# Optimization experiments

Hardware: AMD Instinct MI355X
Metric: run time of the kernel (lower is better)

## Reference

```python
import jax, jax.numpy as jnp
import numpy as np

B, S, D_IN, D_OUT, H = 2, 2048, 1024, 1024, 16
HD = D_OUT // H


def setup_inputs() -> dict:
    key = jax.random.key(0)
    ks = jax.random.split(key, 6)
    s = 0.02
    return {
        "X": jax.random.normal(ks[0], (B, S, D_IN), dtype=jnp.float32),
        "Wq": jax.random.normal(ks[1], (D_OUT, D_IN), dtype=jnp.float32) * s,
        "Wk": jax.random.normal(ks[2], (D_OUT, D_IN), dtype=jnp.float32) * s,
        "Wv": jax.random.normal(ks[3], (D_OUT, D_IN), dtype=jnp.float32) * s,
        "Wo": jax.random.normal(ks[4], (D_OUT, D_OUT), dtype=jnp.float32) * s,
        "bo": jax.random.normal(ks[5], (D_OUT,), dtype=jnp.float32) * s,
    }


def reference(X, Wq, Wk, Wv, Wo, bo):
    b, n, _ = X.shape
    # torch Linear: y = x @ W^T
    Q = (X @ Wq.T).reshape(b, n, H, HD).transpose(0, 2, 1, 3)  # [b,h,s,hd]
    K = (X @ Wk.T).reshape(b, n, H, HD).transpose(0, 2, 1, 3)
    V = (X @ Wv.T).reshape(b, n, H, HD).transpose(0, 2, 1, 3)
    S_ = jnp.einsum('bhqd,bhkd->bhqk', Q, K)  # [b,h,s,s]
    causal = jnp.triu(jnp.ones((n, n), dtype=bool), k=1)
    S_ = jnp.where(causal, -jnp.inf, S_)
    W = jax.nn.softmax(S_ / jnp.sqrt(jnp.float32(HD)), axis=-1)
    Z = jnp.einsum('bhqk,bhkd->bhqd', W, V)
    Z = Z.transpose(0, 2, 1, 3).reshape(b, n, D_OUT)
    return Z @ Wo.T + bo
```

## Files before the change

### kernel.cpp

```cpp
#include <hip/hip_runtime.h>
#include <stdint.h>

typedef __bf16 bf16x8 __attribute__((ext_vector_type(8)));
typedef float  f32x4  __attribute__((ext_vector_type(4)));
typedef unsigned int u32x4 __attribute__((ext_vector_type(4)));

#define S_   2048
#define DM   1024
#define QSCALE 0.18033688011112042f

__device__ __forceinline__ unsigned short f2b(float f) {
    uint32_t u = __builtin_bit_cast(uint32_t, f);
    u += 0x7fffu + ((u >> 16) & 1u);
    return (unsigned short)(u >> 16);
}

__device__ __forceinline__ uint32_t pack2bf(float a, float b) {
    uint32_t ua = __builtin_bit_cast(uint32_t, a) + 0x8000u;
    uint32_t ub = __builtin_bit_cast(uint32_t, b) + 0x8000u;
    return __builtin_amdgcn_perm(ub, ua, 0x07060302);
}

__device__ __forceinline__ void glds16(const void* g, void* l) {
    __builtin_amdgcn_global_load_lds(
        (const __attribute__((address_space(1))) void*)g,
        (__attribute__((address_space(3))) void*)l, 16, 0, 0);
}

__global__ void cvt_all(const float* __restrict__ X,
                        const float* __restrict__ Wq, const float* __restrict__ Wk,
                        const float* __restrict__ Wv,
                        unsigned short* __restrict__ Xb, unsigned short* __restrict__ Wb)
{
    size_t i = ((size_t)blockIdx.x * 256 + threadIdx.x) * 4;
    const float* src;
    unsigned short* dst;
    size_t off;
    if (i < (size_t)4194304) { src = X; dst = Xb; off = i; }
    else {
        size_t j = i - 4194304;
        int sel = (int)(j >> 20);
        off = j & 1048575;
        src = (sel == 0) ? Wq : (sel == 1) ? Wk : Wv;
        dst = Wb + (size_t)sel * 1048576;
    }
    float4 v = *(const float4*)&src[off];
    uint2 o;
    o.x = pack2bf(v.x, v.y);
    o.y = pack2bf(v.z, v.w);
    *(uint2*)&dst[off] = o;
}

__global__ void cvt_wo(const float* __restrict__ Wo, unsigned short* __restrict__ Wob)
{
    size_t i = ((size_t)blockIdx.x * 256 + threadIdx.x) * 4;
    float4 v = *(const float4*)&Wo[i];
    uint2 o;
    o.x = pack2bf(v.x, v.y);
    o.y = pack2bf(v.z, v.w);
    *(uint2*)&Wob[i] = o;
}

__global__ __launch_bounds__(256, 2)
void qkv_gemm(const unsigned short* __restrict__ Xb,
              const unsigned short* __restrict__ Wqb,
              const unsigned short* __restrict__ Wkb,
              const unsigned short* __restrict__ Wvb,
              unsigned short* __restrict__ Qo, unsigned short* __restrict__ Ko,
              unsigned short* __restrict__ Vto)
{
    __shared__ unsigned short Ash[128 * 32];
    __shared__ unsigned short Bsh[128 * 32];

    const int t = threadIdx.x;
    const int lane = t & 63, w = t >> 6;
    const int lcol = lane & 15, quad = lane >> 4;
    const int z = blockIdx.z;
    const int rowBase = ((z == 2) ? blockIdx.x : blockIdx.y) * 128;
    const int colBase = ((z == 2) ? blockIdx.y : blockIdx.x) * 128;
    const unsigned short* aPtr = (z == 2) ? Wvb : Xb;
    const unsigned short* bPtr = (z == 0) ? Wqb : (z == 1) ? Wkb : Xb;
    const int wr = (w >> 1) * 64, wc = (w & 1) * 64;

    f32x4 acc[4][4];
    #pragma unroll
    for (int i = 0; i < 4; ++i)
        #pragma unroll
        for (int j = 0; j < 4; ++j) acc[i][j] = (f32x4){0.f,0.f,0.f,0.f};

    for (int k0 = 0; k0 < DM; k0 += 32) {
        __syncthreads();
        #pragma unroll
        for (int p = 0; p < 2; ++p) {
            int ci = p * 256 + t;
            glds16(&aPtr[(size_t)(rowBase + (ci >> 2)) * DM + k0 + (ci & 3) * 8], &Ash[ci * 8]);
        }
        #pragma unroll
        for (int p = 0; p < 2; ++p) {
            int ci = p * 256 + t;
            glds16(&bPtr[(size_t)(colBase + (ci >> 2)) * DM + k0 + (ci & 3) * 8], &Bsh[ci * 8]);
        }
        __syncthreads();
        bf16x8 af[4], bfr[4];
        #pragma unroll
        for (int i = 0; i < 4; ++i) af[i]  = *(const bf16x8*)&Ash[(wr + i*16 + lcol)*32 + quad*8];
        #pragma unroll
        for (int i = 0; i < 4; ++i) bfr[i] = *(const bf16x8*)&Bsh[(wc + i*16 + lcol)*32 + quad*8];
        #pragma unroll
        for (int i = 0; i < 4; ++i)
            #pragma unroll
            for (int j = 0; j < 4; ++j)
                acc[i][j] = __builtin_amdgcn_mfma_f32_16x16x32_bf16(af[i], bfr[j], acc[i][j], 0, 0, 0);
    }

    unsigned short* Cm = (z == 0) ? Qo : (z == 1) ? Ko : Vto;
    const int ld = (z == 2) ? (S_ * 2) : DM;
    const float sc = (z == 0) ? QSCALE : 1.0f;
    #pragma unroll
    for (int i = 0; i < 4; ++i)
        #pragma unroll
        for (int j = 0; j < 4; ++j)
            #pragma unroll
            for (int r = 0; r < 4; ++r) {
                int row = rowBase + wr + i*16 + quad*4 + r;
                int col = colBase + wc + j*16 + lcol;
                Cm[(size_t)row * ld + col] = f2b(acc[i][j][r] * sc);
            }
}

__global__ __launch_bounds__(512, 4)
void attn_kernel(const unsigned short* __restrict__ Q,
                 const unsigned short* __restrict__ K,
                 const unsigned short* __restrict__ Vt,
                 unsigned short* __restrict__ Z)
{
    __shared__ __align__(16) unsigned short SH[18432];

    const int t = threadIdx.x;
    const int lane = t & 63, w = t >> 6;
    const int lcol = lane & 15, quad = lane >> 4;
    const int kh = w & 1, wq = w >> 1;

    const int bh = blockIdx.x;
    const int b = bh >> 4, h = bh & 15;
    const int y = blockIdx.y;
    const int tile = (y < 8) ? (15 - y) : (y - 8);
    const int q0 = tile * 128;
    const int nchunk = 2 * tile + 2;

    const unsigned short* Qg = Q + (size_t)(b * S_ + q0) * DM + h * 64;
    const unsigned short* Kg = K + (size_t)(b * S_) * DM + h * 64;
    const unsigned short* Vg = Vt + (size_t)(h * 64) * (S_ * 2) + b * S_;

    bf16x8 qf[2][2];
    #pragma unroll
    for (int qi = 0; qi < 2; ++qi)
        #pragma unroll
        for (int kd = 0; kd < 2; ++kd)
            qf[qi][kd] = *(const bf16x8*)&Qg[(size_t)(wq*32 + qi*16 + lcol) * DM + kd*32 + quad*8];

    bool mk[4];
    #pragma unroll
    for (int r = 0; r < 4; ++r) mk[r] = (quad*4 + r) > lcol;

    float lp[2] = {0.f, 0.f};
    f32x4 o[2][4];
    #pragma unroll
    for (int qi = 0; qi < 2; ++qi)
        #pragma unroll
        for (int nd = 0; nd < 4; ++nd) o[qi][nd] = (f32x4){0.f,0.f,0.f,0.f};

    const int sr = t >> 3, sch = t & 7;

    {
        uint4 k0 = *(const uint4*)&Kg[(size_t)sr * DM + sch * 8];
        uint4 v0 = *(const uint4*)&Vg[(size_t)sr * (S_ * 2) + sch * 8];
        *(uint4*)&SH[sr * 72 + sch * 8] = k0;
        *(uint4*)&SH[9216 + sr * 72 + sch * 8] = v0;
    }
    __syncthreads();

    const int Qb0 = tile * 8 + wq * 2;
    const int gq = ((quad & 1) << 1) | (quad >> 1);
    const bool qodd = (quad & 1) != 0;

    for (int c = 0; c < nchunk; ++c) {
        const int cur = c & 1;
        const bool pf = (c + 1 < nchunk);
        uint4 kn, vn;
        if (pf) {
            const int kc1 = (c + 1) * 64;
            kn = *(const uint4*)&Kg[(size_t)(kc1 + sr) * DM + sch * 8];
            vn = *(const uint4*)&Vg[(size_t)sr * (S_ * 2) + kc1 + sch * 8];
        }
        const unsigned short* Kc = &SH[cur * 4608];
        const unsigned short* Vc = &SH[9216 + cur * 4608];

        const int Kb0 = c * 4 + kh * 2;
        if (Kb0 <= Qb0 + 1) {
            uint32_t pw[2][2][2];
            #pragma unroll
            for (int nk = 0; nk < 2; ++nk) {
                const int Kb = Kb0 + nk;
                if (Kb <= Qb0 + 1) {
                    bf16x8 ak0 = *(const bf16x8*)&Kc[(kh*32 + nk*16 + lcol)*72 + quad*8];
                    bf16x8 ak1 = *(const bf16x8*)&Kc[(kh*32 + nk*16 + lcol)*72 + 32 + quad*8];
                    #pragma unroll
                    for (int qi = 0; qi < 2; ++qi) {
                        if (Kb <= Qb0 + qi) {
                            f32x4 s = (f32x4){0.f,0.f,0.f,0.f};
                            s = __builtin_amdgcn_mfma_f32_16x16x32_bf16(ak0, qf[qi][0], s, 0, 0, 0);
                            s = __builtin_amdgcn_mfma_f32_16x16x32_bf16(ak1, qf[qi][1], s, 0, 0, 0);
                            float p0 = __builtin_amdgcn_exp2f(s[0]);
                            float p1 = __builtin_amdgcn_exp2f(s[1]);
                            float p2 = __builtin_amdgcn_exp2f(s[2]);
                            float p3 = __builtin_amdgcn_exp2f(s[3]);
                            if (Kb == Qb0 + qi) {
                                p0 = mk[0] ? 0.f : p0;
                                p1 = mk[1] ? 0.f : p1;
                                p2 = mk[2] ? 0.f : p2;
                                p3 = mk[3] ? 0.f : p3;
                            }
                            lp[qi] += (p0 + p1) + (p2 + p3);
                            pw[qi][nk][0] = pack2bf(p0, p1);
                            pw[qi][nk][1] = pack2bf(p2, p3);
                        } else {
                            pw[qi][nk][0] = 0u;
                            pw[qi][nk][1] = 0u;
                        }
                    }
                } else {
                    #pragma unroll
                    for (int qi = 0; qi < 2; ++qi) {
                        pw[qi][nk][0] = 0u;
                        pw[qi][nk][1] = 0u;
                    }
                }
            }

            bf16x8 ap[2];
            #pragma unroll
            for (int qi = 0; qi < 2; ++qi) {
                uint32_t a0 = pw[qi][0][0], a1 = pw[qi][0][1];
                uint32_t b0 = pw[qi][1][0], b1 = pw[qi][1][1];
                uint32_t xa0 = (uint32_t)__shfl_xor((int)a0, 16);
                uint32_t xa1 = (uint32_t)__shfl_xor((int)a1, 16);
                uint32_t xb0 = (uint32_t)__shfl_xor((int)b0, 16);
                uint32_t xb1 = (uint32_t)__shfl_xor((int)b1, 16);
                u32x4 apw;
                apw[0] = qodd ? xb0 : a0;
                apw[1] = qodd ? xb1 : a1;
                apw[2] = qodd ? b0 : xa0;
                apw[3] = qodd ? b1 : xa1;
                ap[qi] = __builtin_bit_cast(bf16x8, apw);
            }

            #pragma unroll
            for (int nd = 0; nd < 4; ++nd) {
                bf16x8 bv = *(const bf16x8*)&Vc[(nd*16 + lcol)*72 + kh*32 + gq*8];
                #pragma unroll
                for (int qi = 0; qi < 2; ++qi)
                    o[qi][nd] = __builtin_amdgcn_mfma_f32_16x16x32_bf16(ap[qi], bv, o[qi][nd], 0, 0, 0);
            }
        }

        if (pf) {
            *(uint4*)&SH[(cur ^ 1) * 4608 + sr * 72 + sch * 8] = kn;
            *(uint4*)&SH[9216 + (cur ^ 1) * 4608 + sr * 72 + sch * 8] = vn;
        }
        __syncthreads();
    }

    #pragma unroll
    for (int qi = 0; qi < 2; ++qi) {
        lp[qi] += __shfl_xor(lp[qi], 16);
        lp[qi] += __shfl_xor(lp[qi], 32);
    }
    float* red = (float*)SH;
    float* my = red + (wq * 64 + lane) * 36;
    if (kh == 1) {
        #pragma unroll
        for (int qi = 0; qi < 2; ++qi)
            #pragma unroll
            for (int nd = 0; nd < 4; ++nd)
                *(f32x4*)&my[qi*16 + nd*4] = o[qi][nd];
        my[32] = lp[0];
        my[33] = lp[1];
    }
    __syncthreads();
    if (kh == 0) {
        #pragma unroll
        for (int qi = 0; qi < 2; ++qi)
            #pragma unroll
            for (int nd = 0; nd < 4; ++nd)
                o[qi][nd] += *(const f32x4*)&my[qi*16 + nd*4];
        float linv[2];
        linv[0] = 1.0f / (lp[0] + my[32]);
        linv[1] = 1.0f / (lp[1] + my[33]);
        #pragma unroll
        for (int qi = 0; qi < 2; ++qi)
            #pragma unroll
            for (int r = 0; r < 4; ++r) {
                float lr = __shfl(linv[qi], quad*4 + r);
                unsigned short* Zr = Z + (size_t)(b*S_ + q0 + wq*32 + qi*16 + quad*4 + r) * DM + h*64;
                #pragma unroll
                for (int nd = 0; nd < 4; ++nd)
                    Zr[nd*16 + lcol] = f2b(o[qi][nd][r] * lr);
            }
    }
}

__global__ __launch_bounds__(256, 4)
void out_gemm(const unsigned short* __restrict__ A,
              const unsigned short* __restrict__ Wob, const float* __restrict__ bo,
              float* __restrict__ Out)
{
    __shared__ unsigned short Ash[64 * 32];
    __shared__ unsigned short Bsh[128 * 32];

    const int t = threadIdx.x;
    const int lane = t & 63, w = t >> 6;
    const int lcol = lane & 15, quad = lane >> 4;
    const int rowBase = blockIdx.y * 64;
    const int colBase = blockIdx.x * 128;
    const int wr = (w >> 1) * 32, wc = (w & 1) * 64;

    f32x4 acc[2][4];
    #pragma unroll
    for (int i = 0; i < 2; ++i)
        #pragma unroll
        for (int j = 0; j < 4; ++j) acc[i][j] = (f32x4){0.f,0.f,0.f,0.f};

    for (int k0 = 0; k0 < DM; k0 += 32) {
        __syncthreads();
        glds16(&A[(size_t)(rowBase + (t >> 2)) * DM + k0 + (t & 3) * 8], &Ash[t * 8]);
        #pragma unroll
        for (int p = 0; p < 2; ++p) {
            int ci = p * 256 + t;
            glds16(&Wob[(size_t)(colBase + (ci >> 2)) * DM + k0 + (ci & 3) * 8], &Bsh[ci * 8]);
        }
        __syncthreads();
        bf16x8 af[2], bfr[4];
        #pragma unroll
        for (int i = 0; i < 2; ++i) af[i]  = *(const bf16x8*)&Ash[(wr + i*16 + lcol)*32 + quad*8];
        #pragma unroll
        for (int j = 0; j < 4; ++j) bfr[j] = *(const bf16x8*)&Bsh[(wc + j*16 + lcol)*32 + quad*8];
        #pragma unroll
        for (int i = 0; i < 2; ++i)
            #pragma unroll
            for (int j = 0; j < 4; ++j)
                acc[i][j] = __builtin_amdgcn_mfma_f32_16x16x32_bf16(af[i], bfr[j], acc[i][j], 0, 0, 0);
    }

    float bb[4];
    #pragma unroll
    for (int j = 0; j < 4; ++j) bb[j] = bo[colBase + wc + j*16 + lcol];

    #pragma unroll
    for (int i = 0; i < 2; ++i)
        #pragma unroll
        for (int j = 0; j < 4; ++j)
            #pragma unroll
            for (int r = 0; r < 4; ++r) {
                int row = rowBase + wr + i*16 + quad*4 + r;
                int col = colBase + wc + j*16 + lcol;
                Out[(size_t)row * DM + col] = acc[i][j][r] + bb[j];
            }
}

extern "C" void kernel_launch(void* const* d_in, const int* in_sizes, int n_in,
                              void* d_out, int out_size, void* d_ws, size_t ws_size,
                              hipStream_t stream) {
    const float* X  = (const float*)d_in[0];
    const float* Wq = (const float*)d_in[1];
    const float* Wk = (const float*)d_in[2];
    const float* Wv = (const float*)d_in[3];
    const float* Wo = (const float*)d_in[4];
    const float* bo = (const float*)d_in[5];
    float* out = (float*)d_out;

    unsigned short* Xb  = (unsigned short*)d_ws;
    unsigned short* Qw  = Xb + (size_t)4096 * 1024;
    unsigned short* Kw  = Qw + (size_t)4096 * 1024;
    unsigned short* Vtw = Kw + (size_t)4096 * 1024;
    unsigned short* Zb  = Xb;
    unsigned short* Wob = Qw;
    unsigned short* Wb  = (unsigned short*)d_out;

    cvt_all<<<dim3(7168), 256, 0, stream>>>(X, Wq, Wk, Wv, Xb, Wb);
    qkv_gemm<<<dim3(8, 32, 3), 256, 0, stream>>>(Xb, Wb, Wb + (size_t)1048576,
                                                 Wb + (size_t)2097152, Qw, Kw, Vtw);
    attn_kernel<<<dim3(32, 16), 512, 0, stream>>>(Qw, Kw, Vtw, Zb);
    cvt_wo<<<dim3(1024), 256, 0, stream>>>(Wo, Wob);
    out_gemm<<<dim3(8, 64), 256, 0, stream>>>(Zb, Wob, bo, out);
}
```

Baseline: 179.1 us.

## Halve attention query tile to 64 rows and use 16x16x16 MFMA for PV

Shrinks the attention block from 512 to 256 threads with 64-row query tiles, doubling the grid and adjusting the causal chunk count and K/V staging loops. When the 16x16x16 bf16 MFMA builtin is available, the P·V product uses it directly on the packed probability registers, avoiding the cross-lane shuffles that repack P for the 16x16x32 instruction. The aim is better load balance and occupancy on the causal workload with less shuffle overhead. The cost is K/V being reloaded by twice as many blocks and twice as many smaller-K MFMAs.

```diff
diff --git a/kernel.cpp b/kernel.cpp
--- a/kernel.cpp
+++ b/kernel.cpp
@@ -3,6 +3,8 @@
 
 typedef __bf16 bf16x8 __attribute__((ext_vector_type(8)));
 typedef float  f32x4  __attribute__((ext_vector_type(4)));
+typedef short  s16x4  __attribute__((ext_vector_type(4)));
+typedef unsigned int u32x2 __attribute__((ext_vector_type(2)));
 typedef unsigned int u32x4 __attribute__((ext_vector_type(4)));
 
 #define S_   2048
@@ -128,7 +130,13 @@
             }
 }
 
-__global__ __launch_bounds__(512, 4)
+#if __has_builtin(__builtin_amdgcn_mfma_f32_16x16x16bf16_1k)
+#define PV16 1
+#else
+#define PV16 0
+#endif
+
+__global__ __launch_bounds__(256, 4)
 void attn_kernel(const unsigned short* __restrict__ Q,
                  const unsigned short* __restrict__ K,
                  const unsigned short* __restrict__ Vt,
@@ -144,9 +152,9 @@
     const int bh = blockIdx.x;
     const int b = bh >> 4, h = bh & 15;
     const int y = blockIdx.y;
-    const int tile = (y < 8) ? (15 - y) : (y - 8);
-    const int q0 = tile * 128;
-    const int nchunk = 2 * tile + 2;
+    const int tile = (y < 16) ? (31 - y) : (y - 16);
+    const int q0 = tile * 64;
+    const int nchunk = tile + 1;
 
     const unsigned short* Qg = Q + (size_t)(b * S_ + q0) * DM + h * 64;
     const unsigned short* Kg = K + (size_t)(b * S_) * DM + h * 64;
@@ -172,26 +180,34 @@
 
     const int sr = t >> 3, sch = t & 7;
 
-    {
-        uint4 k0 = *(const uint4*)&Kg[(size_t)sr * DM + sch * 8];
-        uint4 v0 = *(const uint4*)&Vg[(size_t)sr * (S_ * 2) + sch * 8];
-        *(uint4*)&SH[sr * 72 + sch * 8] = k0;
-        *(uint4*)&SH[9216 + sr * 72 + sch * 8] = v0;
+    #pragma unroll
+    for (int p = 0; p < 2; ++p) {
+        const int row = p*32 + sr;
+        uint4 k0 = *(const uint4*)&Kg[(size_t)row * DM + sch * 8];
+        uint4 v0 = *(const uint4*)&Vg[(size_t)row * (S_ * 2) + sch * 8];
+        *(uint4*)&SH[row * 72 + sch * 8] = k0;
+        *(uint4*)&SH[9216 + row * 72 + sch * 8] = v0;
     }
     __syncthreads();
 
-    const int Qb0 = tile * 8 + wq * 2;
+    const int Qb0 = tile * 4 + wq * 2;
+#if !PV16
     const int gq = ((quad & 1) << 1) | (quad >> 1);
     const bool qodd = (quad & 1) != 0;
+#endif
 
     for (int c = 0; c < nchunk; ++c) {
         const int cur = c & 1;
         const bool pf = (c + 1 < nchunk);
-        uint4 kn, vn;
+        uint4 kn[2], vn[2];
         if (pf) {
             const int kc1 = (c + 1) * 64;
-            kn = *(const uint4*)&Kg[(size_t)(kc1 + sr) * DM + sch * 8];
-            vn = *(const uint4*)&Vg[(size_t)sr * (S_ * 2) + kc1 + sch * 8];
+            #pragma unroll
+            for (int p = 0; p < 2; ++p) {
+                const int row = p*32 + sr;
+                kn[p] = *(const uint4*)&Kg[(size_t)(kc1 + row) * DM + sch * 8];
+                vn[p] = *(const uint4*)&Vg[(size_t)row * (S_ * 2) + kc1 + sch * 8];
+            }
         }
         const unsigned short* Kc = &SH[cur * 4608];
         const unsigned short* Vc = &SH[9216 + cur * 4608];
@@ -238,6 +254,26 @@
                 }
             }
 
+#if PV16
+            #pragma unroll
+            for (int nk = 0; nk < 2; ++nk) {
+                if (Kb0 + nk <= Qb0 + 1) {
+                    #pragma unroll
+                    for (int nd = 0; nd < 4; ++nd) {
+                        s16x4 bv = *(const s16x4*)&Vc[(nd*16 + lcol)*72 + kh*32 + nk*16 + quad*4];
+                        #pragma unroll
+                        for (int qi = 0; qi < 2; ++qi) {
+                            u32x2 wv;
+                            wv[0] = pw[qi][nk][0];
+                            wv[1] = pw[qi][nk][1];
+                            s16x4 ap = __builtin_bit_cast(s16x4, wv);
+                            o[qi][nd] = __builtin_amdgcn_mfma_f32_16x16x16bf16_1k(
+                                            ap, bv, o[qi][nd], 0, 0, 0);
+                        }
+                    }
+                }
+            }
+#else
             bf16x8 ap[2];
             #pragma unroll
             for (int qi = 0; qi < 2; ++qi) {
@@ -254,7 +290,6 @@
                 apw[3] = qodd ? b1 : xa1;
                 ap[qi] = __builtin_bit_cast(bf16x8, apw);
             }
-
             #pragma unroll
             for (int nd = 0; nd < 4; ++nd) {
                 bf16x8 bv = *(const bf16x8*)&Vc[(nd*16 + lcol)*72 + kh*32 + gq*8];
@@ -262,11 +297,16 @@
                 for (int qi = 0; qi < 2; ++qi)
                     o[qi][nd] = __builtin_amdgcn_mfma_f32_16x16x32_bf16(ap[qi], bv, o[qi][nd], 0, 0, 0);
             }
+#endif
         }
 
         if (pf) {
-            *(uint4*)&SH[(cur ^ 1) * 4608 + sr * 72 + sch * 8] = kn;
-            *(uint4*)&SH[9216 + (cur ^ 1) * 4608 + sr * 72 + sch * 8] = vn;
+            #pragma unroll
+            for (int p = 0; p < 2; ++p) {
+                const int row = p*32 + sr;
+                *(uint4*)&SH[(cur ^ 1) * 4608 + row * 72 + sch * 8] = kn[p];
+                *(uint4*)&SH[9216 + (cur ^ 1) * 4608 + row * 72 + sch * 8] = vn[p];
+            }
         }
         __syncthreads();
     }
@@ -390,7 +430,7 @@
     cvt_all<<<dim3(7168), 256, 0, stream>>>(X, Wq, Wk, Wv, Xb, Wb);
     qkv_gemm<<<dim3(8, 32, 3), 256, 0, stream>>>(Xb, Wb, Wb + (size_t)1048576,
                                                  Wb + (size_t)2097152, Qw, Kw, Vtw);
-    attn_kernel<<<dim3(32, 16), 512, 0, stream>>>(Qw, Kw, Vtw, Zb);
+    attn_kernel<<<dim3(32, 32), 256, 0, stream>>>(Qw, Kw, Vtw, Zb);
     cvt_wo<<<dim3(1024), 256, 0, stream>>>(Wo, Wob);
     out_gemm<<<dim3(8, 64), 256, 0, stream>>>(Zb, Wob, bo, out);
 }
```

New measurement: 217.5 us. 1.21x slower.

## Double attention key chunk size to 128 and add MFMA priority hints

Applied to the files above, without the earlier changes.

The attention kernel now processes 128 keys per chunk instead of 64. Each key-half wave handles four 16-key blocks and splits the PV product into two 32-key passes. This halves the number of loop iterations and block-wide barriers per tile, and LDS use nearly doubles to hold the larger K and V double buffers. s_setprio hints are also wrapped around the MFMA groups, which may reduce occupancy and adds more register pressure from the larger prefetch registers.

```diff
diff --git a/kernel.cpp b/kernel.cpp
--- a/kernel.cpp
+++ b/kernel.cpp
@@ -134,7 +134,7 @@
                  const unsigned short* __restrict__ Vt,
                  unsigned short* __restrict__ Z)
 {
-    __shared__ __align__(16) unsigned short SH[18432];
+    __shared__ __align__(16) unsigned short SH[35840];
 
     const int t = threadIdx.x;
     const int lane = t & 63, w = t >> 6;
@@ -146,7 +146,7 @@
     const int y = blockIdx.y;
     const int tile = (y < 8) ? (15 - y) : (y - 8);
     const int q0 = tile * 128;
-    const int nchunk = 2 * tile + 2;
+    const int nchunk = tile + 1;
 
     const unsigned short* Qg = Q + (size_t)(b * S_ + q0) * DM + h * 64;
     const unsigned short* Kg = K + (size_t)(b * S_) * DM + h * 64;
@@ -171,12 +171,17 @@
         for (int nd = 0; nd < 4; ++nd) o[qi][nd] = (f32x4){0.f,0.f,0.f,0.f};
 
     const int sr = t >> 3, sch = t & 7;
+    const int vr = t >> 4, vch = t & 15;
 
     {
-        uint4 k0 = *(const uint4*)&Kg[(size_t)sr * DM + sch * 8];
-        uint4 v0 = *(const uint4*)&Vg[(size_t)sr * (S_ * 2) + sch * 8];
-        *(uint4*)&SH[sr * 72 + sch * 8] = k0;
-        *(uint4*)&SH[9216 + sr * 72 + sch * 8] = v0;
+        uint4 k0a = *(const uint4*)&Kg[(size_t)sr * DM + sch * 8];
+        uint4 k0b = *(const uint4*)&Kg[(size_t)(64 + sr) * DM + sch * 8];
+        uint4 v0a = *(const uint4*)&Vg[(size_t)vr * (S_ * 2) + vch * 8];
+        uint4 v0b = *(const uint4*)&Vg[(size_t)(32 + vr) * (S_ * 2) + vch * 8];
+        *(uint4*)&SH[sr * 72 + sch * 8] = k0a;
+        *(uint4*)&SH[(64 + sr) * 72 + sch * 8] = k0b;
+        *(uint4*)&SH[18432 + vr * 136 + vch * 8] = v0a;
+        *(uint4*)&SH[18432 + (32 + vr) * 136 + vch * 8] = v0b;
     }
     __syncthreads();
 
@@ -187,86 +192,95 @@
     for (int c = 0; c < nchunk; ++c) {
         const int cur = c & 1;
         const bool pf = (c + 1 < nchunk);
-        uint4 kn, vn;
+        uint4 kn[2], vn[2];
         if (pf) {
-            const int kc1 = (c + 1) * 64;
-            kn = *(const uint4*)&Kg[(size_t)(kc1 + sr) * DM + sch * 8];
-            vn = *(const uint4*)&Vg[(size_t)sr * (S_ * 2) + kc1 + sch * 8];
-        }
-        const unsigned short* Kc = &SH[cur * 4608];
-        const unsigned short* Vc = &SH[9216 + cur * 4608];
-
-        const int Kb0 = c * 4 + kh * 2;
-        if (Kb0 <= Qb0 + 1) {
-            uint32_t pw[2][2][2];
-            #pragma unroll
-            for (int nk = 0; nk < 2; ++nk) {
-                const int Kb = Kb0 + nk;
-                if (Kb <= Qb0 + 1) {
-                    bf16x8 ak0 = *(const bf16x8*)&Kc[(kh*32 + nk*16 + lcol)*72 + quad*8];
-                    bf16x8 ak1 = *(const bf16x8*)&Kc[(kh*32 + nk*16 + lcol)*72 + 32 + quad*8];
-                    #pragma unroll
-                    for (int qi = 0; qi < 2; ++qi) {
-                        if (Kb <= Qb0 + qi) {
-                            f32x4 s = (f32x4){0.f,0.f,0.f,0.f};
-                            s = __builtin_amdgcn_mfma_f32_16x16x32_bf16(ak0, qf[qi][0], s, 0, 0, 0);
-                            s = __builtin_amdgcn_mfma_f32_16x16x32_bf16(ak1, qf[qi][1], s, 0, 0, 0);
-                            float p0 = __builtin_amdgcn_exp2f(s[0]);
-                            float p1 = __builtin_amdgcn_exp2f(s[1]);
-                            float p2 = __builtin_amdgcn_exp2f(s[2]);
-                            float p3 = __builtin_amdgcn_exp2f(s[3]);
-                            if (Kb == Qb0 + qi) {
-                                p0 = mk[0] ? 0.f : p0;
-                                p1 = mk[1] ? 0.f : p1;
-                                p2 = mk[2] ? 0.f : p2;
-                                p3 = mk[3] ? 0.f : p3;
-                            }
-                            lp[qi] += (p0 + p1) + (p2 + p3);
-                            pw[qi][nk][0] = pack2bf(p0, p1);
-                            pw[qi][nk][1] = pack2bf(p2, p3);
-                        } else {
-                            pw[qi][nk][0] = 0u;
-                            pw[qi][nk][1] = 0u;
+            const int kc1 = (c + 1) * 128;
+            kn[0] = *(const uint4*)&Kg[(size_t)(kc1 + sr) * DM + sch * 8];
+            kn[1] = *(const uint4*)&Kg[(size_t)(kc1 + 64 + sr) * DM + sch * 8];
+            vn[0] = *(const uint4*)&Vg[(size_t)vr * (S_ * 2) + kc1 + vch * 8];
+            vn[1] = *(const uint4*)&Vg[(size_t)(32 + vr) * (S_ * 2) + kc1 + vch * 8];
+        }
+        const unsigned short* Kc = &SH[cur * 9216];
+        const unsigned short* Vc = &SH[18432 + cur * 8704];
+
+        const int Kb0 = c * 8 + kh * 4;
+        uint32_t pw[2][4][2];
+        #pragma unroll
+        for (int qi = 0; qi < 2; ++qi)
+            #pragma unroll
+            for (int nk = 0; nk < 4; ++nk) {
+                pw[qi][nk][0] = 0u;
+                pw[qi][nk][1] = 0u;
+            }
+
+        #pragma unroll
+        for (int nk = 0; nk < 4; ++nk) {
+            const int Kb = Kb0 + nk;
+            if (Kb <= Qb0 + 1) {
+                bf16x8 ak0 = *(const bf16x8*)&Kc[(kh*64 + nk*16 + lcol)*72 + quad*8];
+                bf16x8 ak1 = *(const bf16x8*)&Kc[(kh*64 + nk*16 + lcol)*72 + 32 + quad*8];
+                #pragma unroll
+                for (int qi = 0; qi < 2; ++qi) {
+                    if (Kb <= Qb0 + qi) {
+                        f32x4 s = (f32x4){0.f,0.f,0.f,0.f};
+                        __builtin_amdgcn_s_setprio(1);
+                        s = __builtin_amdgcn_mfma_f32_16x16x32_bf16(ak0, qf[qi][0], s, 0, 0, 0);
+                        s = __builtin_amdgcn_mfma_f32_16x16x32_bf16(ak1, qf[qi][1], s, 0, 0, 0);
+                        __builtin_amdgcn_s_setprio(0);
+                        float p0 = __builtin_amdgcn_exp2f(s[0]);
+                        float p1 = __builtin_amdgcn_exp2f(s[1]);
+                        float p2 = __builtin_amdgcn_exp2f(s[2]);
+                        float p3 = __builtin_amdgcn_exp2f(s[3]);
+                        if (Kb == Qb0 + qi) {
+                            p0 = mk[0] ? 0.f : p0;
+                            p1 = mk[1] ? 0.f : p1;
+                            p2 = mk[2] ? 0.f : p2;
+                            p3 = mk[3] ? 0.f : p3;
                         }
-                    }
-                } else {
-                    #pragma unroll
-                    for (int qi = 0; qi < 2; ++qi) {
-                        pw[qi][nk][0] = 0u;
-                        pw[qi][nk][1] = 0u;
+                        lp[qi] += (p0 + p1) + (p2 + p3);
+                        pw[qi][nk][0] = pack2bf(p0, p1);
+                        pw[qi][nk][1] = pack2bf(p2, p3);
                     }
                 }
             }
-
-            bf16x8 ap[2];
-            #pragma unroll
-            for (int qi = 0; qi < 2; ++qi) {
-                uint32_t a0 = pw[qi][0][0], a1 = pw[qi][0][1];
-                uint32_t b0 = pw[qi][1][0], b1 = pw[qi][1][1];
-                uint32_t xa0 = (uint32_t)__shfl_xor((int)a0, 16);
-                uint32_t xa1 = (uint32_t)__shfl_xor((int)a1, 16);
-                uint32_t xb0 = (uint32_t)__shfl_xor((int)b0, 16);
-                uint32_t xb1 = (uint32_t)__shfl_xor((int)b1, 16);
-                u32x4 apw;
-                apw[0] = qodd ? xb0 : a0;
-                apw[1] = qodd ? xb1 : a1;
-                apw[2] = qodd ? b0 : xa0;
-                apw[3] = qodd ? b1 : xa1;
-                ap[qi] = __builtin_bit_cast(bf16x8, apw);
-            }
-
-            #pragma unroll
-            for (int nd = 0; nd < 4; ++nd) {
-                bf16x8 bv = *(const bf16x8*)&Vc[(nd*16 + lcol)*72 + kh*32 + gq*8];
+        }
+
+        #pragma unroll
+        for (int pr = 0; pr < 2; ++pr) {
+            if (Kb0 + 2*pr <= Qb0 + 1) {
+                bf16x8 ap[2];
                 #pragma unroll
-                for (int qi = 0; qi < 2; ++qi)
-                    o[qi][nd] = __builtin_amdgcn_mfma_f32_16x16x32_bf16(ap[qi], bv, o[qi][nd], 0, 0, 0);
+                for (int qi = 0; qi < 2; ++qi) {
+                    uint32_t a0 = pw[qi][2*pr][0], a1 = pw[qi][2*pr][1];
+                    uint32_t b0 = pw[qi][2*pr+1][0], b1 = pw[qi][2*pr+1][1];
+                    uint32_t xa0 = (uint32_t)__shfl_xor((int)a0, 16);
+                    uint32_t xa1 = (uint32_t)__shfl_xor((int)a1, 16);
+                    uint32_t xb0 = (uint32_t)__shfl_xor((int)b0, 16);
+                    uint32_t xb1 = (uint32_t)__shfl_xor((int)b1, 16);
+                    u32x4 apw;
+                    apw[0] = qodd ? xb0 : a0;
+                    apw[1] = qodd ? xb1 : a1;
+                    apw[2] = qodd ? b0 : xa0;
+                    apw[3] = qodd ? b1 : xa1;
+                    ap[qi] = __builtin_bit_cast(bf16x8, apw);
+                }
+                #pragma unroll
+                for (int nd = 0; nd < 4; ++nd) {
+                    bf16x8 bv = *(const bf16x8*)&Vc[(nd*16 + lcol)*136 + kh*64 + pr*32 + gq*8];
+                    __builtin_amdgcn_s_setprio(1);
+                    #pragma unroll
+                    for (int qi = 0; qi < 2; ++qi)
+                        o[qi][nd] = __builtin_amdgcn_mfma_f32_16x16x32_bf16(ap[qi], bv, o[qi][nd], 0, 0, 0);
+                    __builtin_amdgcn_s_setprio(0);
+                }
             }
         }
 
         if (pf) {
-            *(uint4*)&SH[(cur ^ 1) * 4608 + sr * 72 + sch * 8] = kn;
-            *(uint4*)&SH[9216 + (cur ^ 1) * 4608 + sr * 72 + sch * 8] = vn;
+            *(uint4*)&SH[(cur ^ 1) * 9216 + sr * 72 + sch * 8] = kn[0];
+            *(uint4*)&SH[(cur ^ 1) * 9216 + (64 + sr) * 72 + sch * 8] = kn[1];
+            *(uint4*)&SH[18432 + (cur ^ 1) * 8704 + vr * 136 + vch * 8] = vn[0];
+            *(uint4*)&SH[18432 + (cur ^ 1) * 8704 + (32 + vr) * 136 + vch * 8] = vn[1];
         }
         __syncthreads();
     }
```

New measurement: 195.9 us. +9.3%, slower.

## Split long causal attention tiles across two blocks with partial-sum combine kernel

Applied to the files above, without the earlier changes.

Rebalances the causal attention work. Each heavy query tile (tiles 8-15) is split at key chunk 17 between two blocks, and the second block then also processes a light tile (0-7). Unnormalized partial outputs and row sums go to scratch (d_out for outputs, unused rows of Z for sums), and a new combine kernel merges them and normalizes. This evens out per-block work and removes the long-tail blocks, at the cost of an extra launch and the fp32 partial-buffer traffic. No running max is needed because the softmax has no max subtraction.

```diff
diff --git a/kernel.cpp b/kernel.cpp
--- a/kernel.cpp
+++ b/kernel.cpp
@@ -132,7 +132,8 @@
 void attn_kernel(const unsigned short* __restrict__ Q,
                  const unsigned short* __restrict__ K,
                  const unsigned short* __restrict__ Vt,
-                 unsigned short* __restrict__ Z)
+                 unsigned short* __restrict__ Z,
+                 float* __restrict__ Part)
 {
     __shared__ __align__(16) unsigned short SH[18432];
 
@@ -144,169 +145,240 @@
     const int bh = blockIdx.x;
     const int b = bh >> 4, h = bh & 15;
     const int y = blockIdx.y;
-    const int tile = (y < 8) ? (15 - y) : (y - 8);
-    const int q0 = tile * 128;
-    const int nchunk = 2 * tile + 2;
-
-    const unsigned short* Qg = Q + (size_t)(b * S_ + q0) * DM + h * 64;
+    const int ab = y >> 3;
+    const int p = y & 7;
+    const int Hv = 15 - p;
+    const int nH = 2 * Hv + 2;
+
     const unsigned short* Kg = K + (size_t)(b * S_) * DM + h * 64;
     const unsigned short* Vg = Vt + (size_t)(h * 64) * (S_ * 2) + b * S_;
 
-    bf16x8 qf[2][2];
-    #pragma unroll
-    for (int qi = 0; qi < 2; ++qi)
-        #pragma unroll
-        for (int kd = 0; kd < 2; ++kd)
-            qf[qi][kd] = *(const bf16x8*)&Qg[(size_t)(wq*32 + qi*16 + lcol) * DM + kd*32 + quad*8];
-
     bool mk[4];
     #pragma unroll
     for (int r = 0; r < 4; ++r) mk[r] = (quad*4 + r) > lcol;
 
-    float lp[2] = {0.f, 0.f};
-    f32x4 o[2][4];
-    #pragma unroll
-    for (int qi = 0; qi < 2; ++qi)
-        #pragma unroll
-        for (int nd = 0; nd < 4; ++nd) o[qi][nd] = (f32x4){0.f,0.f,0.f,0.f};
-
     const int sr = t >> 3, sch = t & 7;
 
-    {
-        uint4 k0 = *(const uint4*)&Kg[(size_t)sr * DM + sch * 8];
-        uint4 v0 = *(const uint4*)&Vg[(size_t)sr * (S_ * 2) + sch * 8];
-        *(uint4*)&SH[sr * 72 + sch * 8] = k0;
-        *(uint4*)&SH[9216 + sr * 72 + sch * 8] = v0;
-    }
-    __syncthreads();
-
-    const int Qb0 = tile * 8 + wq * 2;
     const int gq = ((quad & 1) << 1) | (quad >> 1);
     const bool qodd = (quad & 1) != 0;
 
-    for (int c = 0; c < nchunk; ++c) {
-        const int cur = c & 1;
-        const bool pf = (c + 1 < nchunk);
-        uint4 kn, vn;
-        if (pf) {
-            const int kc1 = (c + 1) * 64;
-            kn = *(const uint4*)&Kg[(size_t)(kc1 + sr) * DM + sch * 8];
-            vn = *(const uint4*)&Vg[(size_t)sr * (S_ * 2) + kc1 + sch * 8];
-        }
-        const unsigned short* Kc = &SH[cur * 4608];
-        const unsigned short* Vc = &SH[9216 + cur * 4608];
-
-        const int Kb0 = c * 4 + kh * 2;
-        if (Kb0 <= Qb0 + 1) {
-            uint32_t pw[2][2][2];
-            #pragma unroll
-            for (int nk = 0; nk < 2; ++nk) {
-                const int Kb = Kb0 + nk;
-                if (Kb <= Qb0 + 1) {
-                    bf16x8 ak0 = *(const bf16x8*)&Kc[(kh*32 + nk*16 + lcol)*72 + quad*8];
-                    bf16x8 ak1 = *(const bf16x8*)&Kc[(kh*32 + nk*16 + lcol)*72 + 32 + quad*8];
-                    #pragma unroll
-                    for (int qi = 0; qi < 2; ++qi) {
-                        if (Kb <= Qb0 + qi) {
-                            f32x4 s = (f32x4){0.f,0.f,0.f,0.f};
-                            s = __builtin_amdgcn_mfma_f32_16x16x32_bf16(ak0, qf[qi][0], s, 0, 0, 0);
-                            s = __builtin_amdgcn_mfma_f32_16x16x32_bf16(ak1, qf[qi][1], s, 0, 0, 0);
-                            float p0 = __builtin_amdgcn_exp2f(s[0]);
-                            float p1 = __builtin_amdgcn_exp2f(s[1]);
-                            float p2 = __builtin_amdgcn_exp2f(s[2]);
-                            float p3 = __builtin_amdgcn_exp2f(s[3]);
-                            if (Kb == Qb0 + qi) {
-                                p0 = mk[0] ? 0.f : p0;
-                                p1 = mk[1] ? 0.f : p1;
-                                p2 = mk[2] ? 0.f : p2;
-                                p3 = mk[3] ? 0.f : p3;
+    const int nseg = (ab == 0) ? 1 : 2;
+    for (int seg = 0; seg < nseg; ++seg) {
+        int tile, c0, c1;
+        bool finalSeg;
+        if (ab == 0)      { tile = Hv; c0 = 0;  c1 = 17;      finalSeg = false; }
+        else if (seg == 0){ tile = Hv; c0 = 17; c1 = nH;      finalSeg = false; }
+        else              { tile = p;  c0 = 0;  c1 = 2*p + 2; finalSeg = true;  }
+
+        const int q0 = tile * 128;
+        const unsigned short* Qg = Q + (size_t)(b * S_ + q0) * DM + h * 64;
+
+        bf16x8 qf[2][2];
+        #pragma unroll
+        for (int qi = 0; qi < 2; ++qi)
+            #pragma unroll
+            for (int kd = 0; kd < 2; ++kd)
+                qf[qi][kd] = *(const bf16x8*)&Qg[(size_t)(wq*32 + qi*16 + lcol) * DM + kd*32 + quad*8];
+
+        float lp[2] = {0.f, 0.f};
+        f32x4 o[2][4];
+        #pragma unroll
+        for (int qi = 0; qi < 2; ++qi)
+            #pragma unroll
+            for (int nd = 0; nd < 4; ++nd) o[qi][nd] = (f32x4){0.f,0.f,0.f,0.f};
+
+        {
+            const int kc0 = c0 * 64;
+            uint4 k0 = *(const uint4*)&Kg[(size_t)(kc0 + sr) * DM + sch * 8];
+            uint4 v0 = *(const uint4*)&Vg[(size_t)sr * (S_ * 2) + kc0 + sch * 8];
+            *(uint4*)&SH[(c0 & 1) * 4608 + sr * 72 + sch * 8] = k0;
+            *(uint4*)&SH[9216 + (c0 & 1) * 4608 + sr * 72 + sch * 8] = v0;
+        }
+        __syncthreads();
+
+        const int Qb0 = tile * 8 + wq * 2;
+
+        for (int c = c0; c < c1; ++c) {
+            const int cur = c & 1;
+            const bool pf = (c + 1 < c1);
+            uint4 kn, vn;
+            if (pf) {
+                const int kc1 = (c + 1) * 64;
+                kn = *(const uint4*)&Kg[(size_t)(kc1 + sr) * DM + sch * 8];
+                vn = *(const uint4*)&Vg[(size_t)sr * (S_ * 2) + kc1 + sch * 8];
+            }
+            const unsigned short* Kc = &SH[cur * 4608];
+            const unsigned short* Vc = &SH[9216 + cur * 4608];
+
+            const int Kb0 = c * 4 + kh * 2;
+            if (Kb0 <= Qb0 + 1) {
+                uint32_t pw[2][2][2];
+                #pragma unroll
+                for (int nk = 0; nk < 2; ++nk) {
+                    const int Kb = Kb0 + nk;
+                    if (Kb <= Qb0 + 1) {
+                        bf16x8 ak0 = *(const bf16x8*)&Kc[(kh*32 + nk*16 + lcol)*72 + quad*8];
+                        bf16x8 ak1 = *(const bf16x8*)&Kc[(kh*32 + nk*16 + lcol)*72 + 32 + quad*8];
+                        #pragma unroll
+                        for (int qi = 0; qi < 2; ++qi) {
+                            if (Kb <= Qb0 + qi) {
+                                f32x4 s = (f32x4){0.f,0.f,0.f,0.f};
+                                s = __builtin_amdgcn_mfma_f32_16x16x32_bf16(ak0, qf[qi][0], s, 0, 0, 0);
+                                s = __builtin_amdgcn_mfma_f32_16x16x32_bf16(ak1, qf[qi][1], s, 0, 0, 0);
+                                float p0 = __builtin_amdgcn_exp2f(s[0]);
+                                float p1 = __builtin_amdgcn_exp2f(s[1]);
+                                float p2 = __builtin_amdgcn_exp2f(s[2]);
+                                float p3 = __builtin_amdgcn_exp2f(s[3]);
+                                if (Kb == Qb0 + qi) {
+                                    p0 = mk[0] ? 0.f : p0;
+                                    p1 = mk[1] ? 0.f : p1;
+                                    p2 = mk[2] ? 0.f : p2;
+                                    p3 = mk[3] ? 0.f : p3;
+                                }
+                                lp[qi] += (p0 + p1) + (p2 + p3);
+                                pw[qi][nk][0] = pack2bf(p0, p1);
+                                pw[qi][nk][1] = pack2bf(p2, p3);
+                            } else {
+                                pw[qi][nk][0] = 0u;
+                                pw[qi][nk][1] = 0u;
                             }
-                            lp[qi] += (p0 + p1) + (p2 + p3);
-                            pw[qi][nk][0] = pack2bf(p0, p1);
-                            pw[qi][nk][1] = pack2bf(p2, p3);
-                        } else {
+                        }
+                    } else {
+                        #pragma unroll
+                        for (int qi = 0; qi < 2; ++qi) {
                             pw[qi][nk][0] = 0u;
                             pw[qi][nk][1] = 0u;
                         }
                     }
-                } else {
+                }
+
+                bf16x8 ap[2];
+                #pragma unroll
+                for (int qi = 0; qi < 2; ++qi) {
+                    uint32_t a0 = pw[qi][0][0], a1 = pw[qi][0][1];
+                    uint32_t b0 = pw[qi][1][0], b1 = pw[qi][1][1];
+                    uint32_t xa0 = (uint32_t)__shfl_xor((int)a0, 16);
+                    uint32_t xa1 = (uint32_t)__shfl_xor((int)a1, 16);
+                    uint32_t xb0 = (uint32_t)__shfl_xor((int)b0, 16);
+                    uint32_t xb1 = (uint32_t)__shfl_xor((int)b1, 16);
+                    u32x4 apw;
+                    apw[0] = qodd ? xb0 : a0;
+                    apw[1] = qodd ? xb1 : a1;
+                    apw[2] = qodd ? b0 : xa0;
+                    apw[3] = qodd ? b1 : xa1;
+                    ap[qi] = __builtin_bit_cast(bf16x8, apw);
+                }
+
+                #pragma unroll
+                for (int nd = 0; nd < 4; ++nd) {
+                    bf16x8 bv = *(const bf16x8*)&Vc[(nd*16 + lcol)*72 + kh*32 + gq*8];
                     #pragma unroll
-                    for (int qi = 0; qi < 2; ++qi) {
-                        pw[qi][nk][0] = 0u;
-                        pw[qi][nk][1] = 0u;
+                    for (int qi = 0; qi < 2; ++qi)
+                        o[qi][nd] = __builtin_amdgcn_mfma_f32_16x16x32_bf16(ap[qi], bv, o[qi][nd], 0, 0, 0);
+                }
+            }
+
+            if (pf) {
+                *(uint4*)&SH[(cur ^ 1) * 4608 + sr * 72 + sch * 8] = kn;
+                *(uint4*)&SH[9216 + (cur ^ 1) * 4608 + sr * 72 + sch * 8] = vn;
+            }
+            __syncthreads();
+        }
+
+        #pragma unroll
+        for (int qi = 0; qi < 2; ++qi) {
+            lp[qi] += __shfl_xor(lp[qi], 16);
+            lp[qi] += __shfl_xor(lp[qi], 32);
+        }
+        float* red = (float*)SH;
+        float* my = red + (wq * 64 + lane) * 36;
+        if (kh == 1) {
+            #pragma unroll
+            for (int qi = 0; qi < 2; ++qi)
+                #pragma unroll
+                for (int nd = 0; nd < 4; ++nd)
+                    *(f32x4*)&my[qi*16 + nd*4] = o[qi][nd];
+            my[32] = lp[0];
+            my[33] = lp[1];
+        }
+        __syncthreads();
+        if (kh == 0) {
+            #pragma unroll
+            for (int qi = 0; qi < 2; ++qi)
+                #pragma unroll
+                for (int nd = 0; nd < 4; ++nd)
+                    o[qi][nd] += *(const f32x4*)&my[qi*16 + nd*4];
+            float ltot[2];
+            ltot[0] = lp[0] + my[32];
+            ltot[1] = lp[1] + my[33];
+
+            if (finalSeg) {
+                float linv[2];
+                linv[0] = 1.0f / ltot[0];
+                linv[1] = 1.0f / ltot[1];
+                #pragma unroll
+                for (int qi = 0; qi < 2; ++qi)
+                    #pragma unroll
+                    for (int r = 0; r < 4; ++r) {
+                        float lr = __shfl(linv[qi], quad*4 + r);
+                        unsigned short* Zr = Z + (size_t)(b*S_ + q0 + wq*32 + qi*16 + quad*4 + r) * DM + h*64;
+                        #pragma unroll
+                        for (int nd = 0; nd < 4; ++nd)
+                            Zr[nd*16 + lcol] = f2b(o[qi][nd][r] * lr);
                     }
+            } else {
+                float* po = Part + (size_t)(ab ? 2097152 : 0) + (size_t)(bh*8 + p) * 8192;
+                #pragma unroll
+                for (int qi = 0; qi < 2; ++qi)
+                    #pragma unroll
+                    for (int nd = 0; nd < 4; ++nd)
+                        #pragma unroll
+                        for (int r = 0; r < 4; ++r)
+                            po[(wq*32 + qi*16 + quad*4 + r)*64 + nd*16 + lcol] = o[qi][nd][r];
+                if (quad == 0) {
+                    float* st = (float*)(Z + (size_t)(b*S_ + Hv*128 + wq + (ab ? 4 : 0)) * DM + h*64);
+                    st[lcol]      = ltot[0];
+                    st[16 + lcol] = ltot[1];
                 }
             }
-
-            bf16x8 ap[2];
-            #pragma unroll
-            for (int qi = 0; qi < 2; ++qi) {
-                uint32_t a0 = pw[qi][0][0], a1 = pw[qi][0][1];
-                uint32_t b0 = pw[qi][1][0], b1 = pw[qi][1][1];
-                uint32_t xa0 = (uint32_t)__shfl_xor((int)a0, 16);
-                uint32_t xa1 = (uint32_t)__shfl_xor((int)a1, 16);
-                uint32_t xb0 = (uint32_t)__shfl_xor((int)b0, 16);
-                uint32_t xb1 = (uint32_t)__shfl_xor((int)b1, 16);
-                u32x4 apw;
-                apw[0] = qodd ? xb0 : a0;
-                apw[1] = qodd ? xb1 : a1;
-                apw[2] = qodd ? b0 : xa0;
-                apw[3] = qodd ? b1 : xa1;
-                ap[qi] = __builtin_bit_cast(bf16x8, apw);
-            }
-
-            #pragma unroll
-            for (int nd = 0; nd < 4; ++nd) {
-                bf16x8 bv = *(const bf16x8*)&Vc[(nd*16 + lcol)*72 + kh*32 + gq*8];
-                #pragma unroll
-                for (int qi = 0; qi < 2; ++qi)
-                    o[qi][nd] = __builtin_amdgcn_mfma_f32_16x16x32_bf16(ap[qi], bv, o[qi][nd], 0, 0, 0);
-            }
-        }
-
-        if (pf) {
-            *(uint4*)&SH[(cur ^ 1) * 4608 + sr * 72 + sch * 8] = kn;
-            *(uint4*)&SH[9216 + (cur ^ 1) * 4608 + sr * 72 + sch * 8] = vn;
         }
         __syncthreads();
     }
-
-    #pragma unroll
-    for (int qi = 0; qi < 2; ++qi) {
-        lp[qi] += __shfl_xor(lp[qi], 16);
-        lp[qi] += __shfl_xor(lp[qi], 32);
-    }
-    float* red = (float*)SH;
-    float* my = red + (wq * 64 + lane) * 36;
-    if (kh == 1) {
-        #pragma unroll
-        for (int qi = 0; qi < 2; ++qi)
-            #pragma unroll
-            for (int nd = 0; nd < 4; ++nd)
-                *(f32x4*)&my[qi*16 + nd*4] = o[qi][nd];
-        my[32] = lp[0];
-        my[33] = lp[1];
-    }
+}
+
+__global__ __launch_bounds__(256)
+void attn_combine(const float* __restrict__ Part, unsigned short* __restrict__ Z)
+{
+    const int blk = blockIdx.x;
+    const int bh = blk >> 3, p = blk & 7;
+    const int b = bh >> 4, h = bh & 15;
+    const int Hv = 15 - p;
+    const int t = threadIdx.x;
+    const int row = t >> 1, ch = (t & 1) * 32;
+
+    const float* pa = Part + (size_t)blk * 8192;
+    const float* pb = Part + 2097152 + (size_t)blk * 8192;
+
+    const float* stA = (const float*)(Z + (size_t)(b*S_ + Hv*128 + (row >> 5)) * DM + h*64);
+    const float* stB = (const float*)(Z + (size_t)(b*S_ + Hv*128 + 4 + (row >> 5)) * DM + h*64);
+    float lA = stA[row & 31];
+    float lB = stB[row & 31];
     __syncthreads();
-    if (kh == 0) {
-        #pragma unroll
-        for (int qi = 0; qi < 2; ++qi)
-            #pragma unroll
-            for (int nd = 0; nd < 4; ++nd)
-                o[qi][nd] += *(const f32x4*)&my[qi*16 + nd*4];
-        float linv[2];
-        linv[0] = 1.0f / (lp[0] + my[32]);
-        linv[1] = 1.0f / (lp[1] + my[33]);
-        #pragma unroll
-        for (int qi = 0; qi < 2; ++qi)
-            #pragma unroll
-            for (int r = 0; r < 4; ++r) {
-                float lr = __shfl(linv[qi], quad*4 + r);
-                unsigned short* Zr = Z + (size_t)(b*S_ + q0 + wq*32 + qi*16 + quad*4 + r) * DM + h*64;
-                #pragma unroll
-                for (int nd = 0; nd < 4; ++nd)
-                    Zr[nd*16 + lcol] = f2b(o[qi][nd][r] * lr);
-            }
+    float linv = 1.0f / (lA + lB);
+
+    unsigned short* Zr = Z + (size_t)(b*S_ + Hv*128 + row) * DM + h*64;
+    #pragma unroll
+    for (int j = 0; j < 8; ++j) {
+        f32x4 va = *(const f32x4*)&pa[row*64 + ch + j*4];
+        f32x4 vb = *(const f32x4*)&pb[row*64 + ch + j*4];
+        uint2 ozz;
+        float v0 = (va[0] + vb[0]) * linv;
+        float v1 = (va[1] + vb[1]) * linv;
+        float v2 = (va[2] + vb[2]) * linv;
+        float v3 = (va[3] + vb[3]) * linv;
+        ozz.x = pack2bf(v0, v1);
+        ozz.y = pack2bf(v2, v3);
+        *(uint2*)&Zr[ch + j*4] = ozz;
     }
 }
 
@@ -390,7 +462,8 @@
     cvt_all<<<dim3(7168), 256, 0, stream>>>(X, Wq, Wk, Wv, Xb, Wb);
     qkv_gemm<<<dim3(8, 32, 3), 256, 0, stream>>>(Xb, Wb, Wb + (size_t)1048576,
                                                  Wb + (size_t)2097152, Qw, Kw, Vtw);
-    attn_kernel<<<dim3(32, 16), 512, 0, stream>>>(Qw, Kw, Vtw, Zb);
+    attn_kernel<<<dim3(32, 16), 512, 0, stream>>>(Qw, Kw, Vtw, Zb, (float*)d_out);
+    attn_combine<<<dim3(256), 256, 0, stream>>>((const float*)d_out, Zb);
     cvt_wo<<<dim3(1024), 256, 0, stream>>>(Wo, Wob);
     out_gemm<<<dim3(8, 64), 256, 0, stream>>>(Zb, Wob, bo, out);
 }
```

Measured after the change: 185.7 us. 1.04x slower.
